# Optimization experiments

Hardware: AMD Instinct MI355X
Metric: run time of the kernel (lower is better)

## Reference

```python
import jax, jax.numpy as jnp
import numpy as np

N_NODES = 100000
N_EDGES = 1600000
IN_C, HID_C, OUT_C = 128, 256, 128


def setup_inputs() -> dict:
    key = jax.random.key(0)
    ks = jax.random.split(key, 8)
    x = jax.random.normal(ks[0], (N_NODES, IN_C), dtype=jnp.float32)
    edge_row = jax.random.randint(ks[1], (N_EDGES,), 0, N_NODES, dtype=jnp.int32)
    edge_col = jax.random.randint(ks[2], (N_EDGES,), 0, N_NODES, dtype=jnp.int32)
    # normalized adjacency values (e.g. D^-1/2 A D^-1/2 entries), positive
    edge_vals = jax.random.uniform(ks[3], (N_EDGES,), dtype=jnp.float32) * 0.1
    # torch Linear weights: y = x @ W.T + b (xavier scale)
    W1 = jax.random.normal(ks[4], (HID_C, IN_C), dtype=jnp.float32) * (2.0 / (IN_C + HID_C)) ** 0.5
    b1 = jnp.zeros((HID_C,), dtype=jnp.float32)
    W2 = jax.random.normal(ks[5], (HID_C, HID_C), dtype=jnp.float32) * (1.0 / HID_C) ** 0.5
    b2 = jnp.zeros((HID_C,), dtype=jnp.float32)
    W3 = jax.random.normal(ks[6], (OUT_C, HID_C), dtype=jnp.float32) * (2.0 / (HID_C + OUT_C)) ** 0.5
    b3 = jnp.zeros((OUT_C,), dtype=jnp.float32)
    return {"x": x, "edge_row": edge_row, "edge_col": edge_col, "edge_vals": edge_vals,
            "W1": W1, "b1": b1, "W2": W2, "b2": b2, "W3": W3, "b3": b3}


def reference(x, edge_row, edge_col, edge_vals, W1, b1, W2, b2, W3, b3):
    n = x.shape[0]

    def spmm(h):
        # out[i] = sum over edges e with row[e]==i of vals[e] * h[col[e]]
        msgs = h[edge_col] * edge_vals[:, None]          # [E, C]
        return jax.ops.segment_sum(msgs, edge_row, num_segments=n)

    h = jax.nn.relu(spmm(x) @ W1.T + b1)                 # GCNConv 1 + relu
    h = jax.nn.relu(spmm(h) @ W2.T + b2)                 # GCNConv 2 + relu
    h = spmm(h) @ W3.T + b3                              # GCNConv 3 (no act)
    # F.normalize: L2 along dim=1 with eps clamp 1e-12
    norm = jnp.linalg.norm(h, axis=1, keepdims=True)
    return h / jnp.maximum(norm, 1e-12)
```

## Files before the change

kernel.cpp:

```cpp
#include <hip/hip_runtime.h>
#include <hip/hip_bf16.h>

#define N_NODES 100000
#define N_EDGES 1600000
#define IN_C 128
#define HID_C 256
#define OUT_C 128

typedef __attribute__((ext_vector_type(8))) short bf16x8;
typedef __attribute__((ext_vector_type(4))) float f32x4;
typedef __attribute__((ext_vector_type(2))) float f32x2;

static __device__ __forceinline__ short f2bf(float f) {
    union { float f; unsigned u; } x{f};
    unsigned r = (x.u + 0x7fffu + ((x.u >> 16) & 1u)) >> 16;
    return (short)r;
}
static __device__ __forceinline__ f32x2 bfpair(unsigned d) {
    union { unsigned u; float f; } lo, hi;
    lo.u = d << 16;
    hi.u = d & 0xffff0000u;
    return f32x2{lo.f, hi.f};
}

__global__ void hist_rank(const int* __restrict__ rows, int* __restrict__ deg,
                          int* __restrict__ rank, int E)
{
    int e = blockIdx.x * blockDim.x + threadIdx.x;
    if (e < E) rank[e] = atomicAdd(&deg[rows[e]], 1);
}

#define SCAN_BLOCK 256
#define SCAN_ELEMS 1024

__global__ __launch_bounds__(SCAN_BLOCK) void scan1(const int* __restrict__ deg,
                                                    int* __restrict__ excl,
                                                    int* __restrict__ bsum, int N)
{
    __shared__ int sh[SCAN_BLOCK];
    int t = threadIdx.x;
    int base = blockIdx.x * SCAN_ELEMS + t * 4;
    int v[4];
    #pragma unroll
    for (int i = 0; i < 4; ++i) {
        int idx = base + i;
        v[i] = (idx < N) ? deg[idx] : 0;
    }
    int s = v[0] + v[1] + v[2] + v[3];
    sh[t] = s;
    __syncthreads();
    for (int d = 1; d < SCAN_BLOCK; d <<= 1) {
        int add = (t >= d) ? sh[t - d] : 0;
        __syncthreads();
        sh[t] += add;
        __syncthreads();
    }
    int p = sh[t] - s;
    #pragma unroll
    for (int i = 0; i < 4; ++i) {
        int idx = base + i;
        if (idx < N) excl[idx] = p;
        p += v[i];
    }
    if (t == SCAN_BLOCK - 1) bsum[blockIdx.x] = sh[t];
}

__global__ void scan3(int* __restrict__ row_start, const int* __restrict__ bsum,
                      int NB, int N, int E)
{
    __shared__ int pref[128];
    int t = threadIdx.x;
    if (t < 128) pref[t] = (t < NB) ? bsum[t] : 0;
    __syncthreads();
    for (int d = 1; d < 128; d <<= 1) {
        int add = (t < 128 && t >= d) ? pref[t - d] : 0;
        __syncthreads();
        if (t < 128) pref[t] += add;
        __syncthreads();
    }
    int i = blockIdx.x * blockDim.x + t;
    if (i < N) {
        int b = i >> 10;
        row_start[i] += (b == 0) ? 0 : pref[b - 1];
    } else if (i == N) {
        row_start[N] = E;
    }
}

__global__ void scatter_cast(const int* __restrict__ rows, const int* __restrict__ cols,
                             const float* __restrict__ vals, const int* __restrict__ row_start,
                             const int* __restrict__ rank, int2* __restrict__ epk, int E,
                             const float* __restrict__ s0, short* __restrict__ d0, int n0,
                             const float* __restrict__ s1, short* __restrict__ d1, int n1,
                             const float* __restrict__ s2, short* __restrict__ d2, int n2,
                             const float* __restrict__ s3, short* __restrict__ d3, int n3)
{
    int idx = blockIdx.x * blockDim.x + threadIdx.x;
    if (idx < E) {
        int pos = row_start[rows[idx]] + rank[idx];
        epk[pos] = int2{cols[idx], __float_as_int(vals[idx])};
    } else {
        int i = (idx - E) * 4;
        int castN = n0 + n1 + n2 + n3;
        if (i >= castN) return;
        const float* s; short* d;
        if (i < n0) { s = s0; d = d0; }
        else if ((i -= n0) < n1) { s = s1; d = d1; }
        else if ((i -= n1) < n2) { s = s2; d = d2; }
        else { i -= n2; s = s3; d = d3; }
        float4 v = *(const float4*)(s + i);
        *(short4*)(d + i) = short4{f2bf(v.x), f2bf(v.y), f2bf(v.z), f2bf(v.w)};
    }
}

template<int B>
static __device__ __forceinline__ void quad_batch(
    const unsigned* __restrict__ Hb, const int2* __restrict__ epk,
    int j, int sel, int loff, f32x2* acc)
{
    int2 e[B];
    #pragma unroll
    for (int b = 0; b < B; ++b) e[b] = epk[j + 4 * b + sel];
    uint4 g[B];
    #pragma unroll
    for (int b = 0; b < B; ++b)
        g[b] = *(const uint4*)(Hb + (size_t)e[b].x * 64 + loff);
    #pragma unroll
    for (int b = 0; b < B; ++b) {
        const float v = __int_as_float(e[b].y);
        acc[0] += v * bfpair(g[b].x);
        acc[1] += v * bfpair(g[b].y);
        acc[2] += v * bfpair(g[b].z);
        acc[3] += v * bfpair(g[b].w);
    }
}

template<int MODE>
__global__ __launch_bounds__(256) void spmm_gather_q(
    const short* __restrict__ H, const int* __restrict__ row_start,
    const int2* __restrict__ epk, void* __restrict__ outv,
    const float* __restrict__ bias, int N)
{
    const int wid = threadIdx.x >> 6;
    const int lane = threadIdx.x & 63;
    const int sel = lane >> 4;
    const int l15 = lane & 15;
    const int loff = l15 * 4;
    const int row = blockIdx.x * 4 + wid;
    if (row >= N) return;
    int j = row_start[row];
    const int end = row_start[row + 1];
    const unsigned* Hb = (const unsigned*)H;

    f32x2 acc[4] = {};

    for (; j + 16 <= end; j += 16) quad_batch<4>(Hb, epk, j, sel, loff, acc);
    for (; j + 4 <= end; j += 4)   quad_batch<1>(Hb, epk, j, sel, loff, acc);
    if (j < end) {
        const int rem = end - j;
        int2 e = epk[j + (sel < rem ? sel : rem - 1)];
        uint4 g = *(const uint4*)(Hb + (size_t)e.x * 64 + loff);
        const float v = (sel < rem) ? __int_as_float(e.y) : 0.f;
        acc[0] += v * bfpair(g.x);
        acc[1] += v * bfpair(g.y);
        acc[2] += v * bfpair(g.z);
        acc[3] += v * bfpair(g.w);
    }

    #pragma unroll
    for (int u = 0; u < 4; ++u) {
        acc[u].x += __shfl_xor(acc[u].x, 16);
        acc[u].y += __shfl_xor(acc[u].y, 16);
        acc[u].x += __shfl_xor(acc[u].x, 32);
        acc[u].y += __shfl_xor(acc[u].y, 32);
    }

    if constexpr (MODE == 0) {
        if (lane < 16) {
            unsigned od[4];
            #pragma unroll
            for (int u = 0; u < 4; ++u)
                od[u] = (unsigned)(unsigned short)f2bf(acc[u].x)
                      | ((unsigned)(unsigned short)f2bf(acc[u].y) << 16);
            *(uint4*)((unsigned*)outv + (size_t)row * 64 + loff) =
                uint4{od[0], od[1], od[2], od[3]};
        }
    } else {
        const int c0 = l15 * 8;
        float4 b0 = *(const float4*)(bias + c0);
        float4 b1 = *(const float4*)(bias + c0 + 4);
        float o0 = acc[0].x + b0.x, o1 = acc[0].y + b0.y;
        float o2 = acc[1].x + b0.z, o3 = acc[1].y + b0.w;
        float o4 = acc[2].x + b1.x, o5 = acc[2].y + b1.y;
        float o6 = acc[3].x + b1.z, o7 = acc[3].y + b1.w;
        float ss = o0*o0 + o1*o1 + o2*o2 + o3*o3 + o4*o4 + o5*o5 + o6*o6 + o7*o7;
        #pragma unroll
        for (int d = 1; d < 16; d <<= 1)
            ss += __shfl_xor(ss, d);
        float s = 1.0f / fmaxf(sqrtf(ss), 1e-12f);
        if (lane < 16) {
            float* orow = (float*)outv + (size_t)row * 128 + c0;
            *(float4*)orow       = float4{o0 * s, o1 * s, o2 * s, o3 * s};
            *(float4*)(orow + 4) = float4{o4 * s, o5 * s, o6 * s, o7 * s};
        }
    }
}

template<int B>
static __device__ __forceinline__ void pair256_batch(
    const unsigned* __restrict__ Hb, const int2* __restrict__ epk,
    int j, int sel, int loff, f32x2* acc)
{
    int2 e[B];
    #pragma unroll
    for (int b = 0; b < B; ++b) e[b] = epk[j + 2 * b + sel];
    uint4 g[B];
    #pragma unroll
    for (int b = 0; b < B; ++b)
        g[b] = *(const uint4*)(Hb + (size_t)e[b].x * 128 + loff);
    #pragma unroll
    for (int b = 0; b < B; ++b) {
        const float v = __int_as_float(e[b].y);
        acc[0] += v * bfpair(g[b].x);
        acc[1] += v * bfpair(g[b].y);
        acc[2] += v * bfpair(g[b].z);
        acc[3] += v * bfpair(g[b].w);
    }
}

__global__ __launch_bounds__(256) void spmm_gather_p256(
    const short* __restrict__ H, const int* __restrict__ row_start,
    const int2* __restrict__ epk, void* __restrict__ outv, int N)
{
    const int wid = threadIdx.x >> 6;
    const int lane = threadIdx.x & 63;
    const int sel = lane >> 5;
    const int l31 = lane & 31;
    const int loff = l31 * 4;
    const int row = blockIdx.x * 4 + wid;
    if (row >= N) return;
    int j = row_start[row];
    const int end = row_start[row + 1];
    const unsigned* Hb = (const unsigned*)H;

    f32x2 acc[4] = {};

    for (; j + 8 <= end; j += 8) pair256_batch<4>(Hb, epk, j, sel, loff, acc);
    for (; j + 2 <= end; j += 2) pair256_batch<1>(Hb, epk, j, sel, loff, acc);
    if (j < end) {
        int2 e = epk[j];
        uint4 g = *(const uint4*)(Hb + (size_t)e.x * 128 + loff);
        const float v = sel ? 0.f : __int_as_float(e.y);
        acc[0] += v * bfpair(g.x);
        acc[1] += v * bfpair(g.y);
        acc[2] += v * bfpair(g.z);
        acc[3] += v * bfpair(g.w);
    }

    #pragma unroll
    for (int u = 0; u < 4; ++u) {
        acc[u].x += __shfl_xor(acc[u].x, 32);
        acc[u].y += __shfl_xor(acc[u].y, 32);
    }

    if (lane < 32) {
        unsigned od[4];
        #pragma unroll
        for (int u = 0; u < 4; ++u)
            od[u] = (unsigned)(unsigned short)f2bf(acc[u].x)
                  | ((unsigned)(unsigned short)f2bf(acc[u].y) << 16);
        *(uint4*)((unsigned*)outv + (size_t)row * 128 + loff) =
            uint4{od[0], od[1], od[2], od[3]};
    }
}

template<int K, int M, bool RELU, bool BIAS>
__global__ __launch_bounds__(256) void gemm_bf16(
    const short* __restrict__ A, const short* __restrict__ W,
    const float* __restrict__ bias, short* __restrict__ Y, int N)
{
    constexpr int MBLK = M / 64;
    constexpr int BK = 32;
    constexpr int PAD = 8;
    __shared__ short As[128][BK + PAD];
    __shared__ short Ws[64][BK + PAD];

    const int id = blockIdx.x;
    const int bx = (id / (8 * MBLK)) * 8 + (id & 7);
    const int by = (id >> 3) & (MBLK - 1);

    const int tid = threadIdx.x;
    const int wid = tid >> 6;
    const int lane = tid & 63;
    const int wm = wid & 1;
    const int wn = wid >> 1;
    const int l15 = lane & 15;
    const int quad = lane >> 4;
    const int bn = bx * 128;
    const int bm = by * 64;

    f32x4 acc[4][2] = {};

    for (int k0 = 0; k0 < K; k0 += BK) {
        #pragma unroll
        for (int c = 0; c < 2; ++c) {
            int chunk = tid + c * 256;
            int row = chunk >> 2;
            int koff = (chunk & 3) * 8;
            int gr = bn + row;
            ulonglong2 v = {0ull, 0ull};
            if (gr < N) v = *(const ulonglong2*)(A + (size_t)gr * K + k0 + koff);
            *(ulonglong2*)&As[row][koff] = v;
        }
        {
            int row = tid >> 2;
            int koff = (tid & 3) * 8;
            ulonglong2 v = *(const ulonglong2*)(W + (size_t)(bm + row) * K + k0 + koff);
            *(ulonglong2*)&Ws[row][koff] = v;
        }
        __syncthreads();

        bf16x8 aF[4], bF[2];
        #pragma unroll
        for (int mt = 0; mt < 4; ++mt)
            aF[mt] = *(const bf16x8*)&As[wm * 64 + mt * 16 + l15][quad * 8];
        #pragma unroll
        for (int nt = 0; nt < 2; ++nt)
            bF[nt] = *(const bf16x8*)&Ws[wn * 32 + nt * 16 + l15][quad * 8];

        #pragma unroll
        for (int mt = 0; mt < 4; ++mt)
            #pragma unroll
            for (int nt = 0; nt < 2; ++nt)
                acc[mt][nt] = __builtin_amdgcn_mfma_f32_16x16x32_bf16(
                    aF[mt], bF[nt], acc[mt][nt], 0, 0, 0);
        __syncthreads();
    }

    #pragma unroll
    for (int nt = 0; nt < 2; ++nt) {
        int col = bm + wn * 32 + nt * 16 + l15;
        float bv = BIAS ? bias[col] : 0.f;
        #pragma unroll
        for (int mt = 0; mt < 4; ++mt) {
            int row0 = bn + wm * 64 + mt * 16 + quad * 4;
            #pragma unroll
            for (int r = 0; r < 4; ++r) {
                int row = row0 + r;
                if (row < N) {
                    float v = acc[mt][nt][r] + bv;
                    if (RELU) v = fmaxf(v, 0.f);
                    Y[(size_t)row * M + col] = f2bf(v);
                }
            }
        }
    }
}

extern "C" void kernel_launch(void* const* d_in, const int* in_sizes, int n_in,
                              void* d_out, int out_size, void* d_ws, size_t ws_size,
                              hipStream_t stream) {
    const float* x        = (const float*)d_in[0];
    const int*   edge_row = (const int*)d_in[1];
    const int*   edge_col = (const int*)d_in[2];
    const float* edge_val = (const float*)d_in[3];
    const float* W1       = (const float*)d_in[4];
    const float* b1       = (const float*)d_in[5];
    const float* W2       = (const float*)d_in[6];
    const float* b2       = (const float*)d_in[7];
    const float* W3       = (const float*)d_in[8];
    const float* b3       = (const float*)d_in[9];
    float* out = (float*)d_out;

    const int N = N_NODES, E = N_EDGES;
    const int NB = (N + SCAN_ELEMS - 1) / SCAN_ELEMS;

    short* xbf = (short*)d_ws;
    short* Hbf = xbf + (size_t)N * IN_C;
    short* Gbf = Hbf + (size_t)N * HID_C;
    short* W1b = Gbf + (size_t)N * HID_C;
    short* W2b = W1b + HID_C * IN_C;
    short* W3b = W2b + HID_C * HID_C;
    int* deg = (int*)(((uintptr_t)(W3b + OUT_C * HID_C) + 15) & ~(uintptr_t)15);
    int* row_start = deg + N;
    int* rank      = row_start + (N + 1);
    int* bsum      = rank + E;
    int2* epk      = (int2*)(((uintptr_t)(bsum + 128) + 15) & ~(uintptr_t)15);

    hipMemsetAsync(deg, 0, N * sizeof(int), stream);
    hist_rank<<<(E + 255) / 256, 256, 0, stream>>>(edge_row, deg, rank, E);
    scan1<<<NB, SCAN_BLOCK, 0, stream>>>(deg, row_start, bsum, N);
    scan3<<<(N + 256) / 256, 256, 0, stream>>>(row_start, bsum, NB, N, E);
    {
        int n0 = N * IN_C, n1 = HID_C * IN_C, n2 = HID_C * HID_C, n3 = OUT_C * HID_C;
        int total = E + (n0 + n1 + n2 + n3) / 4;
        scatter_cast<<<(total + 255) / 256, 256, 0, stream>>>(
            edge_row, edge_col, edge_val, row_start, rank, epk, E,
            x, xbf, n0, W1, W1b, n1, W2, W2b, n2, W3, W3b, n3);
    }

    const int spmm_grid = (N + 3) / 4;
    const int GXP = ((N + 127) / 128 + 7) & ~7;

    spmm_gather_q<0><<<spmm_grid, 256, 0, stream>>>(
        xbf, row_start, epk, Hbf, nullptr, N);
    gemm_bf16<IN_C, HID_C, true, true><<<GXP * (HID_C / 64), 256, 0, stream>>>(
        Hbf, W1b, b1, Gbf, N);

    spmm_gather_p256<<<spmm_grid, 256, 0, stream>>>(
        Gbf, row_start, epk, Hbf, N);
    gemm_bf16<HID_C, HID_C, true, true><<<GXP * (HID_C / 64), 256, 0, stream>>>(
        Hbf, W2b, b2, Gbf, N);

    gemm_bf16<HID_C, OUT_C, false, false><<<GXP * (OUT_C / 64), 256, 0, stream>>>(
        Gbf, W3b, nullptr, Hbf, N);
    spmm_gather_q<2><<<spmm_grid, 256, 0, stream>>>(
        Hbf, row_start, epk, out, b3, N);
}
```

Before: 562.9 us.

## Privatize degree histogram per XCC and fuse bf16 cast into histogram kernel

The degree histogram is split into eight per-XCC copies, selected by reading the hardware XCC_ID register, so atomics from different dies hit separate memory. The scan then folds the eight copies into per-XCC offsets, and the scatter adds these offsets to build CSR positions. The float-to-bf16 casts of x and the weights move from the scatter kernel into the histogram kernel. This adds an 8x larger memset and extra scan reads and writes in exchange for less cross-die atomic contention, and it relies on the XCC id being at most 7 and on per-XCC ranks fitting in 24 bits.

```diff
diff --git a/kernel.cpp b/kernel.cpp
--- a/kernel.cpp
+++ b/kernel.cpp
@@ -23,82 +23,21 @@
     return f32x2{lo.f, hi.f};
 }
 
-__global__ void hist_rank(const int* __restrict__ rows, int* __restrict__ deg,
-                          int* __restrict__ rank, int E)
-{
-    int e = blockIdx.x * blockDim.x + threadIdx.x;
-    if (e < E) rank[e] = atomicAdd(&deg[rows[e]], 1);
-}
-
-#define SCAN_BLOCK 256
-#define SCAN_ELEMS 1024
-
-__global__ __launch_bounds__(SCAN_BLOCK) void scan1(const int* __restrict__ deg,
-                                                    int* __restrict__ excl,
-                                                    int* __restrict__ bsum, int N)
-{
-    __shared__ int sh[SCAN_BLOCK];
-    int t = threadIdx.x;
-    int base = blockIdx.x * SCAN_ELEMS + t * 4;
-    int v[4];
-    #pragma unroll
-    for (int i = 0; i < 4; ++i) {
-        int idx = base + i;
-        v[i] = (idx < N) ? deg[idx] : 0;
-    }
-    int s = v[0] + v[1] + v[2] + v[3];
-    sh[t] = s;
-    __syncthreads();
-    for (int d = 1; d < SCAN_BLOCK; d <<= 1) {
-        int add = (t >= d) ? sh[t - d] : 0;
-        __syncthreads();
-        sh[t] += add;
-        __syncthreads();
-    }
-    int p = sh[t] - s;
-    #pragma unroll
-    for (int i = 0; i < 4; ++i) {
-        int idx = base + i;
-        if (idx < N) excl[idx] = p;
-        p += v[i];
-    }
-    if (t == SCAN_BLOCK - 1) bsum[blockIdx.x] = sh[t];
-}
-
-__global__ void scan3(int* __restrict__ row_start, const int* __restrict__ bsum,
-                      int NB, int N, int E)
-{
-    __shared__ int pref[128];
-    int t = threadIdx.x;
-    if (t < 128) pref[t] = (t < NB) ? bsum[t] : 0;
-    __syncthreads();
-    for (int d = 1; d < 128; d <<= 1) {
-        int add = (t < 128 && t >= d) ? pref[t - d] : 0;
-        __syncthreads();
-        if (t < 128) pref[t] += add;
-        __syncthreads();
-    }
-    int i = blockIdx.x * blockDim.x + t;
-    if (i < N) {
-        int b = i >> 10;
-        row_start[i] += (b == 0) ? 0 : pref[b - 1];
-    } else if (i == N) {
-        row_start[N] = E;
-    }
-}
-
-__global__ void scatter_cast(const int* __restrict__ rows, const int* __restrict__ cols,
-                             const float* __restrict__ vals, const int* __restrict__ row_start,
-                             const int* __restrict__ rank, int2* __restrict__ epk, int E,
-                             const float* __restrict__ s0, short* __restrict__ d0, int n0,
-                             const float* __restrict__ s1, short* __restrict__ d1, int n1,
-                             const float* __restrict__ s2, short* __restrict__ d2, int n2,
-                             const float* __restrict__ s3, short* __restrict__ d3, int n3)
+__global__ void hist_rank_cast(const int* __restrict__ rows, int* __restrict__ degx,
+                               int* __restrict__ rank, int E,
+                               const float* __restrict__ s0, short* __restrict__ d0, int n0,
+                               const float* __restrict__ s1, short* __restrict__ d1, int n1,
+                               const float* __restrict__ s2, short* __restrict__ d2, int n2,
+                               const float* __restrict__ s3, short* __restrict__ d3, int n3)
 {
     int idx = blockIdx.x * blockDim.x + threadIdx.x;
     if (idx < E) {
-        int pos = row_start[rows[idx]] + rank[idx];
-        epk[pos] = int2{cols[idx], __float_as_int(vals[idx])};
+        unsigned xcc;
+        asm volatile("s_getreg_b32 %0, hwreg(HW_REG_XCC_ID)" : "=s"(xcc));
+        xcc &= 7u;
+        int r = rows[idx];
+        int rl = atomicAdd(&degx[xcc * N_NODES + r], 1);
+        rank[idx] = (int)((xcc << 24) | (unsigned)rl);
     } else {
         int i = (idx - E) * 4;
         int castN = n0 + n1 + n2 + n3;
@@ -111,6 +50,87 @@
         float4 v = *(const float4*)(s + i);
         *(short4*)(d + i) = short4{f2bf(v.x), f2bf(v.y), f2bf(v.z), f2bf(v.w)};
     }
+}
+
+#define SCAN_BLOCK 256
+#define SCAN_ELEMS 1024
+
+__global__ __launch_bounds__(SCAN_BLOCK) void scan1(int* __restrict__ degx,
+                                                    int* __restrict__ excl,
+                                                    int* __restrict__ bsum, int N)
+{
+    __shared__ int sh[SCAN_BLOCK];
+    int t = threadIdx.x;
+    int base = blockIdx.x * SCAN_ELEMS + t * 4;
+    int v[4];
+    #pragma unroll
+    for (int i = 0; i < 4; ++i) {
+        int idx = base + i;
+        int s8 = 0;
+        if (idx < N) {
+            #pragma unroll
+            for (int x = 0; x < 8; ++x) {
+                int c = degx[x * N_NODES + idx];
+                degx[x * N_NODES + idx] = s8;
+                s8 += c;
+            }
+        }
+        v[i] = s8;
+    }
+    int s = v[0] + v[1] + v[2] + v[3];
+    sh[t] = s;
+    __syncthreads();
+    for (int d = 1; d < SCAN_BLOCK; d <<= 1) {
+        int add = (t >= d) ? sh[t - d] : 0;
+        __syncthreads();
+        sh[t] += add;
+        __syncthreads();
+    }
+    int p = sh[t] - s;
+    #pragma unroll
+    for (int i = 0; i < 4; ++i) {
+        int idx = base + i;
+        if (idx < N) excl[idx] = p;
+        p += v[i];
+    }
+    if (t == SCAN_BLOCK - 1) bsum[blockIdx.x] = sh[t];
+}
+
+__global__ void scan3(int* __restrict__ row_start, const int* __restrict__ bsum,
+                      int NB, int N, int E)
+{
+    __shared__ int pref[128];
+    int t = threadIdx.x;
+    if (t < 128) pref[t] = (t < NB) ? bsum[t] : 0;
+    __syncthreads();
+    for (int d = 1; d < 128; d <<= 1) {
+        int add = (t < 128 && t >= d) ? pref[t - d] : 0;
+        __syncthreads();
+        if (t < 128) pref[t] += add;
+        __syncthreads();
+    }
+    int i = blockIdx.x * blockDim.x + t;
+    if (i < N) {
+        int b = i >> 10;
+        row_start[i] += (b == 0) ? 0 : pref[b - 1];
+    } else if (i == N) {
+        row_start[N] = E;
+    }
+}
+
+__global__ void scatter_epk(const int* __restrict__ rows, const int* __restrict__ cols,
+                            const float* __restrict__ vals, const int* __restrict__ row_start,
+                            const int* __restrict__ degx, const int* __restrict__ rank,
+                            int2* __restrict__ epk, int E)
+{
+    int idx = blockIdx.x * blockDim.x + threadIdx.x;
+    if (idx >= E) return;
+    int rk = rank[idx];
+    int x  = (int)(((unsigned)rk) >> 24);
+    int rl = rk & 0xFFFFFF;
+    int r  = rows[idx];
+    int pos = row_start[r] + degx[x * N_NODES + r] + rl;
+    epk[pos] = int2{cols[idx], __float_as_int(vals[idx])};
 }
 
 template<int B>
@@ -381,23 +401,24 @@
     short* W1b = Gbf + (size_t)N * HID_C;
     short* W2b = W1b + HID_C * IN_C;
     short* W3b = W2b + HID_C * HID_C;
-    int* deg = (int*)(((uintptr_t)(W3b + OUT_C * HID_C) + 15) & ~(uintptr_t)15);
-    int* row_start = deg + N;
+    int* degx = (int*)(((uintptr_t)(W3b + OUT_C * HID_C) + 15) & ~(uintptr_t)15);
+    int* row_start = degx + 8 * (size_t)N;
     int* rank      = row_start + (N + 1);
     int* bsum      = rank + E;
     int2* epk      = (int2*)(((uintptr_t)(bsum + 128) + 15) & ~(uintptr_t)15);
 
-    hipMemsetAsync(deg, 0, N * sizeof(int), stream);
-    hist_rank<<<(E + 255) / 256, 256, 0, stream>>>(edge_row, deg, rank, E);
-    scan1<<<NB, SCAN_BLOCK, 0, stream>>>(deg, row_start, bsum, N);
-    scan3<<<(N + 256) / 256, 256, 0, stream>>>(row_start, bsum, NB, N, E);
+    hipMemsetAsync(degx, 0, 8 * (size_t)N * sizeof(int), stream);
     {
         int n0 = N * IN_C, n1 = HID_C * IN_C, n2 = HID_C * HID_C, n3 = OUT_C * HID_C;
         int total = E + (n0 + n1 + n2 + n3) / 4;
-        scatter_cast<<<(total + 255) / 256, 256, 0, stream>>>(
-            edge_row, edge_col, edge_val, row_start, rank, epk, E,
+        hist_rank_cast<<<(total + 255) / 256, 256, 0, stream>>>(
+            edge_row, degx, rank, E,
             x, xbf, n0, W1, W1b, n1, W2, W2b, n2, W3, W3b, n3);
     }
+    scan1<<<NB, SCAN_BLOCK, 0, stream>>>(degx, row_start, bsum, N);
+    scan3<<<(N + 256) / 256, 256, 0, stream>>>(row_start, bsum, NB, N, E);
+    scatter_epk<<<(E + 255) / 256, 256, 0, stream>>>(
+        edge_row, edge_col, edge_val, row_start, degx, rank, epk, E);
 
     const int spmm_grid = (N + 3) / 4;
     const int GXP = ((N + 127) / 128 + 7) & ~7;
```

After: 575.6 us. 1.02x slower.
